# Kernel tuning notes

Measured on AMD Instinct MI355X. Metric: run time of the kernel, lower is better.

The kernel has to match this reference:

```python
import jax, jax.numpy as jnp
import numpy as np

TEMPERATURE = 0.07
MARGIN = 0.2
EPS = 1e-8  # matches torch F.cosine_similarity eps


def _cosine_matrix(a, b):
    # a: (N, D), b: (M, D) -> (N, M) pairwise cosine similarity
    an = a / jnp.clip(jnp.linalg.norm(a, axis=-1, keepdims=True), EPS)
    bn = b / jnp.clip(jnp.linalg.norm(b, axis=-1, keepdims=True), EPS)
    return an @ bn.T


def setup_inputs() -> dict:
    key = jax.random.key(0)
    k1, k2, k3 = jax.random.split(key, 3)
    return {
        "step_embeddings": jax.random.normal(k1, (8192, 1024), dtype=jnp.float32),
        "modal_embeddings": jax.random.normal(k2, (4096, 1024), dtype=jnp.float32),
        "negative_modal_embeddings": jax.random.normal(k3, (4096, 1024), dtype=jnp.float32),
    }


def reference(step_embeddings, modal_embeddings, negative_modal_embeddings):
    # --- step-modal alignment (max cosine sim per step, averaged) ---
    S = _cosine_matrix(step_embeddings, modal_embeddings)        # (N, M)
    per_step = S.max(axis=1)                                      # (N,)
    alignment = per_step.mean()

    # --- attention-weighted alignment (use_attention=True) ---
    logits = (step_embeddings @ modal_embeddings.T) / TEMPERATURE  # (N, M)
    attention = jax.nn.softmax(logits, axis=1)
    weighted_alignment = (S * attention).sum(axis=1).mean()

    # --- contrastive coherence against negatives ---
    Sn = _cosine_matrix(step_embeddings, negative_modal_embeddings)
    negative_alignment = Sn.max(axis=1).mean()
    positive_alignment = alignment
    contrastive_score = positive_alignment - negative_alignment
    margin_score = jax.nn.relu(contrastive_score - MARGIN)

    # --- per-step coherence (same max-cosine per step) ---
    min_step_coherence = per_step.min()

    # overall uses weighted_alignment (attention on), mixed with contrastive
    overall = 0.7 * weighted_alignment + 0.3 * contrastive_score

    return (alignment, weighted_alignment, attention, contrastive_score,
            margin_score, positive_alignment, negative_alignment,
            per_step, min_step_coherence, overall)
```

## Files before the change

kernel.cpp:

```cpp
#include <hip/hip_runtime.h>
#include <cmath>


#define WAVE 64

typedef __bf16 bf16x8_t __attribute__((ext_vector_type(8)));
typedef __bf16 bf16x4_t __attribute__((ext_vector_type(4)));
typedef float f32x4_t __attribute__((ext_vector_type(4)));

__device__ __forceinline__ float wave_reduce_sum(float v) {
#pragma unroll
    for (int o = 32; o > 0; o >>= 1) v += __shfl_down(v, o, WAVE);
    return v;
}
__device__ __forceinline__ float wave_reduce_max(float v) {
#pragma unroll
    for (int o = 32; o > 0; o >>= 1) v = fmaxf(v, __shfl_down(v, o, WAVE));
    return v;
}
__device__ __forceinline__ float wave_reduce_min(float v) {
#pragma unroll
    for (int o = 32; o > 0; o >>= 1) v = fminf(v, __shfl_down(v, o, WAVE));
    return v;
}

__device__ __forceinline__ unsigned enc_f(float f) {
    unsigned u = __float_as_uint(f);
    return (u & 0x80000000u) ? ~u : (u | 0x80000000u);
}
__device__ __forceinline__ float dec_f(unsigned e) {
    unsigned u = (e & 0x80000000u) ? (e & 0x7fffffffu) : ~e;
    return __uint_as_float(u);
}

__global__ __launch_bounds__(256)
void convert_norms_kernel(const float* __restrict__ step,
                          const float* __restrict__ modal,
                          const float* __restrict__ negs,
                          char* __restrict__ arena,
                          float* __restrict__ ina, float* __restrict__ inb,
                          float* __restrict__ inn,
                          unsigned* __restrict__ negmax_u, int N, int M) {
    const int tid = threadIdx.x, lane = tid & 63, wv = tid >> 6;
    const int b = blockIdx.x * 4 + wv;
    const float* src;
    if (b < N)          src = step  + (size_t)b * 1024;
    else if (b < N + M) src = modal + (size_t)(b - N) * 1024;
    else                src = negs  + (size_t)(b - N - M) * 1024;

    char* cb = arena + (((size_t)(b >> 2)) << 14) + ((size_t)(b & 3) << 11) + 8192;
    float s = 0.0f;
#pragma unroll
    for (int q = 0; q < 4; q++) {
        const int idx = lane + q * 64;
        const float4 v = ((const float4*)src)[idx];
        bf16x4_t o;
        o[0] = (__bf16)v.x; o[1] = (__bf16)v.y;
        o[2] = (__bf16)v.z; o[3] = (__bf16)v.w;
        *(bf16x4_t*)(cb + (size_t)idx * 8) = o;
        s += v.x * v.x + v.y * v.y + v.z * v.z + v.w * v.w;
    }
    s = wave_reduce_sum(s);
    if (lane == 0) {
        const float inv = 1.0f / fmaxf(sqrtf(s), 1e-8f);
        if (b < N)          { ina[b] = inv; negmax_u[b] = 0u; }
        else if (b < N + M) inb[b - N] = inv;
        else                inn[b - N - M] = inv;
    }
}

#define GLD16(g, l)                                                        \
    __builtin_amdgcn_global_load_lds(                                     \
        (const __attribute__((address_space(1))) void*)(g),               \
        (__attribute__((address_space(3))) void*)(l), 16, 0, 0)

__global__ __launch_bounds__(256, 4)
void gemm_fused_kernel(char* __restrict__ arena, int N, int M,
                       const float* __restrict__ inv_nn,
                       unsigned* __restrict__ negmax_u) {
    __shared__ __bf16 As[128 * 64];
    __shared__ __bf16 Bs[128 * 64];

    const int lin = blockIdx.x;
    const int st  = lin >> 7;
    const int r128 = lin & 127;
    const int bxi = (st & 7) * 8 + (r128 & 7);
    const int byi = (st >> 3) * 16 + (r128 >> 3);
    const int bm = byi * 128, bn = bxi * 128;

    const int t = threadIdx.x, w = t >> 6, lane = t & 63;
    const int lane16 = lane & 15, lq = lane >> 4;
    const int wm = (w & 1) * 64, wn = (w >> 1) * 64;

    const int s_is_b  = w >> 1;
    const int rowbase = (w & 1) * 64;
    const int ln3 = lane >> 3;
    const int q_g = (lane & 7) ^ ln3;
    const int cbase = (s_is_b ? (N + bn) : bm) + rowbase;
    const int cc = cbase + ln3;
    const size_t off0 = (((size_t)(cc >> 2)) << 14) +
                        ((size_t)(cc & 3) << 11) + 8192 + (size_t)q_g * 16;
    const char* gbase = arena + off0;
    __bf16* ldsw = (s_is_b ? Bs : As) + rowbase * 64;

    f32x4_t acc[4][4];
#pragma unroll
    for (int i = 0; i < 4; i++)
#pragma unroll
        for (int j = 0; j < 4; j++) acc[i][j] = (f32x4_t){0.f, 0.f, 0.f, 0.f};

    const int sxr = lane16 & 7;

    for (int k0b = 0; k0b < 2048; k0b += 128) {
        __syncthreads();
#pragma unroll
        for (int r = 0; r < 8; r++)
            GLD16(gbase + (size_t)r * 32768 + k0b, ldsw + r * 512);
        __syncthreads();

#pragma unroll
        for (int kk = 0; kk < 2; kk++) {
            const int qo = ((lq + kk * 4) ^ sxr) * 8;
            bf16x8_t af[4], bf[4];
#pragma unroll
            for (int i = 0; i < 4; i++)
                af[i] = *(const bf16x8_t*)&As[(wm + i * 16 + lane16) * 64 + qo];
#pragma unroll
            for (int j = 0; j < 4; j++)
                bf[j] = *(const bf16x8_t*)&Bs[(wn + j * 16 + lane16) * 64 + qo];
#pragma unroll
            for (int i = 0; i < 4; i++)
#pragma unroll
                for (int j = 0; j < 4; j++)
                    acc[i][j] = __builtin_amdgcn_mfma_f32_16x16x32_bf16(
                        af[i], bf[j], acc[i][j], 0, 0, 0);
        }
    }

    if (bn < M) {
#pragma unroll
        for (int i = 0; i < 4; i++) {
#pragma unroll
            for (int r = 0; r < 4; r++) {
                const int grow = bm + wm + i * 16 + lq * 4 + r;
                __bf16* dst = (__bf16*)(arena + ((size_t)grow << 14)) +
                              bn + wn + lane16;
#pragma unroll
                for (int j = 0; j < 4; j++)
                    dst[j * 16] = (__bf16)acc[i][j][r];
            }
        }
    } else {
        float invn[4];
#pragma unroll
        for (int j = 0; j < 4; j++)
            invn[j] = inv_nn[(bn - M) + wn + j * 16 + lane16];
#pragma unroll
        for (int i = 0; i < 4; i++) {
#pragma unroll
            for (int r = 0; r < 4; r++) {
                float v = acc[i][0][r] * invn[0];
                v = fmaxf(v, acc[i][1][r] * invn[1]);
                v = fmaxf(v, acc[i][2][r] * invn[2]);
                v = fmaxf(v, acc[i][3][r] * invn[3]);
#pragma unroll
                for (int o = 8; o > 0; o >>= 1)
                    v = fmaxf(v, __shfl_xor(v, o, WAVE));
                if (lane16 == 0)
                    atomicMax(&negmax_u[bm + wm + i * 16 + lq * 4 + r], enc_f(v));
            }
        }
    }
}

#define CUT 2.0f
#define MAXCAND 64

__global__ __launch_bounds__(256)
void softmax_fix_kernel(char* __restrict__ arena, const float* __restrict__ step,
                        const float* __restrict__ modal,
                        const float* __restrict__ ina, const float* __restrict__ inb,
                        float* __restrict__ perstep, float* __restrict__ wout,
                        float* __restrict__ attn) {
    const int row = blockIdx.x, tid = threadIdx.x;
    const int lane = tid & 63, wv = tid >> 6;

    __shared__ float srow_s[1024];
    __shared__ float red[8];
    __shared__ float bcast[2];
    __shared__ int   cand[MAXCAND];
    __shared__ float exact[MAXCAND];
    __shared__ int   cnt;

    if (tid == 0) cnt = 0;
    ((float4*)srow_s)[tid] = ((const float4*)(step + (size_t)row * 1024))[tid];

    const __bf16* gb = (const __bf16*)(arena + ((size_t)row << 14)) + tid * 16;
    float vals[16];
    {
        bf16x8_t v0 = *(const bf16x8_t*)gb;
        bf16x8_t v1 = *(const bf16x8_t*)(gb + 8);
#pragma unroll
        for (int j = 0; j < 8; j++) { vals[j] = (float)v0[j]; vals[8 + j] = (float)v1[j]; }
    }
    float invn[16];
    {
        const float4* p = (const float4*)(inb + tid * 16);
#pragma unroll
        for (int q = 0; q < 4; q++) {
            const float4 x = p[q];
            invn[q * 4 + 0] = x.x; invn[q * 4 + 1] = x.y;
            invn[q * 4 + 2] = x.z; invn[q * 4 + 3] = x.w;
        }
    }

    float dmax = -3.4e38f;
#pragma unroll
    for (int j = 0; j < 16; j++) dmax = fmaxf(dmax, vals[j]);
    float wm = wave_reduce_max(dmax);
    if (lane == 0) red[wv] = wm;
    __syncthreads();
    if (tid == 0) bcast[0] = fmaxf(fmaxf(red[0], red[1]), fmaxf(red[2], red[3]));
    __syncthreads();
    const float m0 = bcast[0];

    const float thr = m0 - CUT;
#pragma unroll
    for (int j = 0; j < 16; j++) {
        if (vals[j] >= thr) {
            const int pos = atomicAdd(&cnt, 1);
            if (pos < MAXCAND) cand[pos] = tid * 16 + j;
        }
    }
    __syncthreads();
    const int nc = min(cnt, MAXCAND);

    for (int i = wv; i < nc; i += 4) {
        const float* mrow = modal + (size_t)cand[i] * 1024;
        float p = 0.0f;
#pragma unroll
        for (int q = 0; q < 16; q++) {
            const int idx = lane + q * 64;
            p = fmaf(srow_s[idx], mrow[idx], p);
        }
        p = wave_reduce_sum(p);
        if (lane == 0) exact[i] = p;
    }
    __syncthreads();

    for (int i = 0; i < nc; i++) {
        const int c = cand[i];
        if ((c >> 4) == tid) vals[c & 15] = exact[i];
    }

    float dmax2 = -3.4e38f, cmax = -3.4e38f;
#pragma unroll
    for (int j = 0; j < 16; j++) {
        dmax2 = fmaxf(dmax2, vals[j]);
        cmax = fmaxf(cmax, vals[j] * invn[j]);
    }
    float wg = wave_reduce_max(dmax2);
    float wc = wave_reduce_max(cmax);
    if (lane == 0) { red[wv] = wg; red[4 + wv] = wc; }
    __syncthreads();
    if (tid == 0) {
        bcast[0] = fmaxf(fmaxf(red[0], red[1]), fmaxf(red[2], red[3]));
        bcast[1] = fmaxf(fmaxf(red[4], red[5]), fmaxf(red[6], red[7]));
    }
    __syncthreads();
    const float invT = 1.0f / 0.07f;
    const float mlog = bcast[0] * invT;
    const float cmaxAll = bcast[1];

    float evals[16];
    float lsum = 0.0f;
#pragma unroll
    for (int j = 0; j < 16; j++) {
        const float e = __expf(vals[j] * invT - mlog);
        evals[j] = e;
        lsum += e;
    }
    lsum = wave_reduce_sum(lsum);
    __syncthreads();
    if (lane == 0) red[wv] = lsum;
    __syncthreads();
    if (tid == 0) bcast[0] = red[0] + red[1] + red[2] + red[3];
    __syncthreads();
    const float invZ = 1.0f / bcast[0];

    float* g32 = attn + (size_t)row * 4096 + tid * 16;
    float wacc = 0.0f;
#pragma unroll
    for (int q = 0; q < 4; q++) {
        float4 o;
        float a0 = evals[q * 4 + 0] * invZ, a1 = evals[q * 4 + 1] * invZ;
        float a2 = evals[q * 4 + 2] * invZ, a3 = evals[q * 4 + 3] * invZ;
        o.x = a0; o.y = a1; o.z = a2; o.w = a3;
        ((float4*)g32)[q] = o;
        wacc += a0 * vals[q * 4 + 0] * invn[q * 4 + 0];
        wacc += a1 * vals[q * 4 + 1] * invn[q * 4 + 1];
        wacc += a2 * vals[q * 4 + 2] * invn[q * 4 + 2];
        wacc += a3 * vals[q * 4 + 3] * invn[q * 4 + 3];
    }
    wacc = wave_reduce_sum(wacc);
    __syncthreads();
    if (lane == 0) red[wv] = wacc;
    __syncthreads();
    if (tid == 0) {
        const float inv_na = ina[row];
        perstep[row] = cmaxAll * inv_na;
        wout[row] = (red[0] + red[1] + red[2] + red[3]) * inv_na;
    }
}

__global__ __launch_bounds__(1024)
void finalize_kernel(const float* __restrict__ perstep, const float* __restrict__ w,
                     const unsigned* __restrict__ negmax_u,
                     const float* __restrict__ ina, float* __restrict__ out,
                     int N, size_t NM) {
    float s_a = 0.0f, s_w = 0.0f, s_n = 0.0f, mn = 3.4e38f;
    for (int i = threadIdx.x; i < N; i += 1024) {
        const float p = perstep[i];
        s_a += p;
        s_w += w[i];
        s_n += dec_f(negmax_u[i]) * ina[i];
        mn = fminf(mn, p);
    }
    s_a = wave_reduce_sum(s_a);
    s_w = wave_reduce_sum(s_w);
    s_n = wave_reduce_sum(s_n);
    mn  = wave_reduce_min(mn);
    __shared__ float ra[16], rw[16], rn[16], rm[16];
    const int lane = threadIdx.x & 63, wv = threadIdx.x >> 6;
    if (lane == 0) { ra[wv] = s_a; rw[wv] = s_w; rn[wv] = s_n; rm[wv] = mn; }
    __syncthreads();
    if (threadIdx.x == 0) {
        float ta = 0, tw = 0, tn = 0, tm = 3.4e38f;
#pragma unroll
        for (int i = 0; i < 16; i++) {
            ta += ra[i]; tw += rw[i]; tn += rn[i]; tm = fminf(tm, rm[i]);
        }
        const float inv = 1.0f / (float)N;
        const float alignment = ta * inv;
        const float weighted  = tw * inv;
        const float neg       = tn * inv;
        const float contrast  = alignment - neg;
        const float margin    = fmaxf(contrast - 0.2f, 0.0f);
        const float overall   = 0.7f * weighted + 0.3f * contrast;
        out[0] = alignment;
        out[1] = weighted;
        float* p = out + 2 + NM;
        p[0] = contrast;
        p[1] = margin;
        p[2] = alignment;
        p[3] = neg;
        p[4 + N] = tm;
        p[5 + N] = overall;
    }
}

extern "C" void kernel_launch(void* const* d_in, const int* in_sizes, int n_in,
                              void* d_out, int out_size, void* d_ws, size_t ws_size,
                              hipStream_t stream) {
    const float* step  = (const float*)d_in[0];
    const float* modal = (const float*)d_in[1];
    const float* negs  = (const float*)d_in[2];
    float* out = (float*)d_out;

    const int K = 1024;
    const int N = in_sizes[0] / K;
    const int M = in_sizes[1] / K;
    const size_t NM = (size_t)N * (size_t)M;

    float* ina        = (float*)d_ws;
    float* inb        = ina + N;
    float* inn        = inb + M;
    unsigned* negmax  = (unsigned*)(inn + M);
    float* wsum       = (float*)(negmax + N);

    char* arena    = (char*)d_out + 16;
    float* attn    = out + 2;
    float* perstep = out + 2 + NM + 4;

    convert_norms_kernel<<<(N + 2 * M) / 4, 256, 0, stream>>>(
        step, modal, negs, arena, ina, inb, inn, negmax, N, M);

    const int nblocks = (N / 128) * ((2 * M) / 128);
    gemm_fused_kernel<<<nblocks, 256, 0, stream>>>(arena, N, M, inn, negmax);

    softmax_fix_kernel<<<N, 256, 0, stream>>>(arena, step, modal, ina, inb,
                                              perstep, wsum, attn);

    finalize_kernel<<<1, 1024, 0, stream>>>(perstep, wsum, negmax, ina, out, N, NM);
}
```

Before: 418.2 us.

## Double-buffer GEMM LDS tiles and coalesce softmax row accesses

The GEMM kernel now uses two LDS buffers per operand and issues the async global-to-LDS loads for the next K-slab while MFMAs consume the current one. A single explicit waitcnt-plus-barrier per iteration replaces the two __syncthreads, which is meant to hide global load latency behind compute. The cost is double the LDS footprint, with launch bounds lowered from 4 to 2 blocks per CU. Separately, the softmax kernel switches from each thread owning 16 contiguous columns to interleaved 4-column groups strided by 1024, so loads of scores and inverse norms and stores of attention are coalesced across threads; candidate index mapping is updated to match.

```diff
diff --git a/kernel.cpp b/kernel.cpp
--- a/kernel.cpp
+++ b/kernel.cpp
@@ -74,12 +74,15 @@
         (const __attribute__((address_space(1))) void*)(g),               \
         (__attribute__((address_space(3))) void*)(l), 16, 0, 0)
 
-__global__ __launch_bounds__(256, 4)
+#define PIPE_BARRIER() asm volatile(                                       \
+    "s_waitcnt vmcnt(0) lgkmcnt(0)\n\ts_barrier" ::: "memory")
+
+__global__ __launch_bounds__(256, 2)
 void gemm_fused_kernel(char* __restrict__ arena, int N, int M,
                        const float* __restrict__ inv_nn,
                        unsigned* __restrict__ negmax_u) {
-    __shared__ __bf16 As[128 * 64];
-    __shared__ __bf16 Bs[128 * 64];
+    __shared__ __bf16 As[2][128 * 64];
+    __shared__ __bf16 Bs[2][128 * 64];
 
     const int lin = blockIdx.x;
     const int st  = lin >> 7;
@@ -101,7 +104,9 @@
     const size_t off0 = (((size_t)(cc >> 2)) << 14) +
                         ((size_t)(cc & 3) << 11) + 8192 + (size_t)q_g * 16;
     const char* gbase = arena + off0;
-    __bf16* ldsw = (s_is_b ? Bs : As) + rowbase * 64;
+    const int ldsoff = rowbase * 64;
+    __bf16* ldsw0 = (s_is_b ? Bs[0] : As[0]) + ldsoff;
+    __bf16* ldsw1 = (s_is_b ? Bs[1] : As[1]) + ldsoff;
 
     f32x4_t acc[4][4];
 #pragma unroll
@@ -111,30 +116,42 @@
 
     const int sxr = lane16 & 7;
 
-    for (int k0b = 0; k0b < 2048; k0b += 128) {
-        __syncthreads();
-#pragma unroll
-        for (int r = 0; r < 8; r++)
-            GLD16(gbase + (size_t)r * 32768 + k0b, ldsw + r * 512);
-        __syncthreads();
-
+#pragma unroll
+    for (int r = 0; r < 8; r++)
+        GLD16(gbase + (size_t)r * 32768, ldsw0 + r * 512);
+
+    for (int it = 0; it < 16; ++it) {
+        PIPE_BARRIER();
+        const int cur = it & 1;
+
+        bf16x8_t af[2][4], bf[2][4];
 #pragma unroll
         for (int kk = 0; kk < 2; kk++) {
             const int qo = ((lq + kk * 4) ^ sxr) * 8;
-            bf16x8_t af[4], bf[4];
 #pragma unroll
             for (int i = 0; i < 4; i++)
-                af[i] = *(const bf16x8_t*)&As[(wm + i * 16 + lane16) * 64 + qo];
+                af[kk][i] = *(const bf16x8_t*)&As[cur][(wm + i * 16 + lane16) * 64 + qo];
 #pragma unroll
             for (int j = 0; j < 4; j++)
-                bf[j] = *(const bf16x8_t*)&Bs[(wn + j * 16 + lane16) * 64 + qo];
+                bf[kk][j] = *(const bf16x8_t*)&Bs[cur][(wn + j * 16 + lane16) * 64 + qo];
+        }
+
+        if (it + 1 < 16) {
+            const size_t k0b = (size_t)(it + 1) * 128;
+            __bf16* ldsw = cur ? ldsw0 : ldsw1;
+#pragma unroll
+            for (int r = 0; r < 8; r++)
+                GLD16(gbase + (size_t)r * 32768 + k0b, ldsw + r * 512);
+        }
+
+#pragma unroll
+        for (int kk = 0; kk < 2; kk++)
 #pragma unroll
             for (int i = 0; i < 4; i++)
 #pragma unroll
                 for (int j = 0; j < 4; j++)
                     acc[i][j] = __builtin_amdgcn_mfma_f32_16x16x32_bf16(
-                        af[i], bf[j], acc[i][j], 0, 0, 0);
-        }
+                        af[kk][i], bf[kk][j], acc[i][j], 0, 0, 0);
     }
 
     if (bn < M) {
@@ -195,23 +212,17 @@
     if (tid == 0) cnt = 0;
     ((float4*)srow_s)[tid] = ((const float4*)(step + (size_t)row * 1024))[tid];
 
-    const __bf16* gb = (const __bf16*)(arena + ((size_t)row << 14)) + tid * 16;
+    const __bf16* gb = (const __bf16*)(arena + ((size_t)row << 14));
     float vals[16];
-    {
-        bf16x8_t v0 = *(const bf16x8_t*)gb;
-        bf16x8_t v1 = *(const bf16x8_t*)(gb + 8);
-#pragma unroll
-        for (int j = 0; j < 8; j++) { vals[j] = (float)v0[j]; vals[8 + j] = (float)v1[j]; }
-    }
     float invn[16];
-    {
-        const float4* p = (const float4*)(inb + tid * 16);
-#pragma unroll
-        for (int q = 0; q < 4; q++) {
-            const float4 x = p[q];
-            invn[q * 4 + 0] = x.x; invn[q * 4 + 1] = x.y;
-            invn[q * 4 + 2] = x.z; invn[q * 4 + 3] = x.w;
-        }
+#pragma unroll
+    for (int g = 0; g < 4; g++) {
+        const bf16x4_t v = *(const bf16x4_t*)(gb + g * 1024 + tid * 4);
+        const float4 x = *(const float4*)(inb + g * 1024 + tid * 4);
+        vals[g * 4 + 0] = (float)v[0]; vals[g * 4 + 1] = (float)v[1];
+        vals[g * 4 + 2] = (float)v[2]; vals[g * 4 + 3] = (float)v[3];
+        invn[g * 4 + 0] = x.x; invn[g * 4 + 1] = x.y;
+        invn[g * 4 + 2] = x.z; invn[g * 4 + 3] = x.w;
     }
 
     float dmax = -3.4e38f;
@@ -226,12 +237,14 @@
 
     const float thr = m0 - CUT;
 #pragma unroll
-    for (int j = 0; j < 16; j++) {
-        if (vals[j] >= thr) {
-            const int pos = atomicAdd(&cnt, 1);
-            if (pos < MAXCAND) cand[pos] = tid * 16 + j;
-        }
-    }
+    for (int g = 0; g < 4; g++)
+#pragma unroll
+        for (int u = 0; u < 4; u++) {
+            if (vals[g * 4 + u] >= thr) {
+                const int pos = atomicAdd(&cnt, 1);
+                if (pos < MAXCAND) cand[pos] = g * 1024 + tid * 4 + u;
+            }
+        }
     __syncthreads();
     const int nc = min(cnt, MAXCAND);
 
@@ -250,7 +263,7 @@
 
     for (int i = 0; i < nc; i++) {
         const int c = cand[i];
-        if ((c >> 4) == tid) vals[c & 15] = exact[i];
+        if (((c & 1023) >> 2) == tid) vals[(c >> 10) * 4 + (c & 3)] = exact[i];
     }
 
     float dmax2 = -3.4e38f, cmax = -3.4e38f;
@@ -288,19 +301,19 @@
     __syncthreads();
     const float invZ = 1.0f / bcast[0];
 
-    float* g32 = attn + (size_t)row * 4096 + tid * 16;
+    float* arow = attn + (size_t)row * 4096;
     float wacc = 0.0f;
 #pragma unroll
-    for (int q = 0; q < 4; q++) {
+    for (int g = 0; g < 4; g++) {
         float4 o;
-        float a0 = evals[q * 4 + 0] * invZ, a1 = evals[q * 4 + 1] * invZ;
-        float a2 = evals[q * 4 + 2] * invZ, a3 = evals[q * 4 + 3] * invZ;
+        const float a0 = evals[g * 4 + 0] * invZ, a1 = evals[g * 4 + 1] * invZ;
+        const float a2 = evals[g * 4 + 2] * invZ, a3 = evals[g * 4 + 3] * invZ;
         o.x = a0; o.y = a1; o.z = a2; o.w = a3;
-        ((float4*)g32)[q] = o;
-        wacc += a0 * vals[q * 4 + 0] * invn[q * 4 + 0];
-        wacc += a1 * vals[q * 4 + 1] * invn[q * 4 + 1];
-        wacc += a2 * vals[q * 4 + 2] * invn[q * 4 + 2];
-        wacc += a3 * vals[q * 4 + 3] * invn[q * 4 + 3];
+        *(float4*)(arow + g * 1024 + tid * 4) = o;
+        wacc += a0 * vals[g * 4 + 0] * invn[g * 4 + 0];
+        wacc += a1 * vals[g * 4 + 1] * invn[g * 4 + 1];
+        wacc += a2 * vals[g * 4 + 2] * invn[g * 4 + 2];
+        wacc += a3 * vals[g * 4 + 3] * invn[g * 4 + 3];
     }
     wacc = wave_reduce_sum(wacc);
     __syncthreads();
```

Result: faster. 398.9 us (-4.6%).
